# Optimization experiments

Hardware: AMD Instinct MI355X
Metric: run time of the kernel (lower is better)

## Reference

```python
import jax, jax.numpy as jnp
import numpy as np

B, S, D, K, NS = 4, 2048, 768, 8192, 2
TAU = 1.0


def setup_inputs() -> dict:
    key = jax.random.key(0)
    k1, k2, k3, k4 = jax.random.split(key, 4)
    x = jax.random.normal(k1, (B, S, D), dtype=jnp.float32)
    w_codebook = jax.random.normal(k2, (K, D), dtype=jnp.float32) * (1.0 / np.sqrt(D))
    embeddings = jax.random.normal(k3, (K, D), dtype=jnp.float32)
    # standard Gumbel(0,1) noise, one draw per (token, sample, code)
    gumbel_noise = jax.random.gumbel(k4, (B, S, NS, K), dtype=jnp.float32)
    return {"x": x, "w_codebook": w_codebook, "embeddings": embeddings,
            "gumbel_noise": gumbel_noise, "num_samples": NS}


def reference(x, w_codebook, embeddings, gumbel_noise, num_samples):
    # logits = Linear(x) without bias: [B, S, K]
    logits = jnp.einsum('bsd,kd->bsk', x, w_codebook)
    # expand over num_samples and add Gumbel noise (F.gumbel_softmax, training)
    g = (logits[:, :, None, :] + gumbel_noise) / TAU          # [B, S, NS, K]
    y_soft = jax.nn.softmax(g, axis=-1)
    # hard one-hot with straight-through estimator (hard=True, hard_p=1.0)
    idx = jnp.argmax(y_soft, axis=-1)                          # [B, S, NS]
    y_hard = jax.nn.one_hot(idx, K, dtype=y_soft.dtype)
    indices = y_hard + y_soft - jax.lax.stop_gradient(y_soft)  # [B, S, NS, K]
    # one-hot matmul == gather of codebook rows
    emb = jnp.einsum('bsnk,kd->bsnd', indices, embeddings)     # [B, S, NS, D]
    return emb, indices
```

## Files before the change

kernel.cpp:

```cpp
#include <hip/hip_runtime.h>
#include <stdint.h>

#define Bc 4
#define Sc 2048
#define Dc 768
#define Kc 8192
#define NSc 2
#define Mc (Bc*Sc)
#define EMB_ELEMS ((size_t)Mc*NSc*Dc)

typedef __attribute__((ext_vector_type(8))) __bf16 bf16x8;
typedef __attribute__((ext_vector_type(4))) float f32x4;
typedef __attribute__((ext_vector_type(4))) unsigned short u16x4;
typedef __attribute__((ext_vector_type(8))) unsigned short u16x8;

__device__ __forceinline__ unsigned short f2bf(float f){
  unsigned int u = __float_as_uint(f);
  u += 0x7FFFu + ((u >> 16) & 1u);
  return (unsigned short)(u >> 16);
}
__device__ __forceinline__ float bf2f(unsigned short h){
  return __uint_as_float(((unsigned int)h) << 16);
}

__global__ __launch_bounds__(256) void k_convert(const float4* __restrict__ x,
                                                 const float4* __restrict__ w,
                                                 u16x4* __restrict__ xb,
                                                 u16x4* __restrict__ wb){
  int i = blockIdx.x * 256 + threadIdx.x;
  float4 v = x[i];
  u16x4 o;
  o.x = f2bf(v.x); o.y = f2bf(v.y); o.z = f2bf(v.z); o.w = f2bf(v.w);
  xb[i] = o;
  v = w[i];
  o.x = f2bf(v.x); o.y = f2bf(v.y); o.z = f2bf(v.z); o.w = f2bf(v.w);
  wb[i] = o;
}

#define BM 128
#define BN 128
#define BK 32

__global__ __launch_bounds__(512, 2) void k_gemm(const unsigned short* __restrict__ xb,
                                                 const unsigned short* __restrict__ wb,
                                                 unsigned short* __restrict__ stash){
  __shared__ __align__(16) unsigned char lds[131072];

  const int tid  = threadIdx.x;
  const int lane = tid & 63;
  const int wid  = tid >> 6;
  const int wr   = wid >> 2;
  const int wc   = wid & 3;
  const int fr   = lane & 15;
  const int fq   = lane >> 4;

  const int bid = (int)blockIdx.x;
  const int swz = (bid & 7) * 128 + (bid >> 3);
  const int bm0 = (swz >> 5) * 256;
  const int bn0 = (swz & 31) * 256;

  f32x4 acc[8][4] = {};

  const int rin   = tid >> 3;
  const int kblkp = (tid & 7) ^ (rin & 7);
  const unsigned short* gsrc[8];
  unsigned dstoff[8];
  #pragma unroll
  for (int s = 0; s < 8; ++s) {
    const int isA = s >> 2;
    const int q   = s & 3;
    const int r64 = isA ? (((q & 1) << 1) | (q >> 1)) : q;
    const int grow = (isA ? bm0 : bn0) + r64 * 64 + rin;
    gsrc[s]   = (isA ? xb : wb) + (size_t)grow * Dc + kblkp * 8;
    dstoff[s] = (isA ? 0u : 32768u) + (unsigned)r64 * 8192u + (unsigned)wid * 1024u;
  }

#define ISSUE(s_, bo_) __builtin_amdgcn_global_load_lds( \
    (const __attribute__((address_space(1))) void*)gsrc[s_], \
    (__attribute__((address_space(3))) void*)&lds[(bo_) + dstoff[s_]], 16, 0, 0)

  #pragma unroll
  for (int s = 0; s < 8; ++s) ISSUE(s, 0u);
  #pragma unroll
  for (int s = 0; s < 8; ++s) gsrc[s] += 64;

  unsigned bufR = 0u, bufW = 65536u;
  const unsigned aRow = (unsigned)(wr*128 + fr) * 128u;
  const unsigned bRow = (unsigned)(wc*64  + fr) * 128u + 32768u;
  const unsigned sl0  = (unsigned)((fq       ) ^ (fr & 7)) * 16u;
  const unsigned sl1  = (unsigned)((fq + 4   ) ^ (fr & 7)) * 16u;

  for (int t = 0; t < 12; ++t) {
    const bool more = (t < 11);
    bf16x8 a[4], b0[4], b1[4];

    asm volatile("s_waitcnt vmcnt(2)" ::: "memory");
    __builtin_amdgcn_s_barrier();
    asm volatile("" ::: "memory");
    if (more) { ISSUE(0, bufW); ISSUE(1, bufW); }
    #pragma unroll
    for (int n = 0; n < 4; ++n) b0[n] = *(const bf16x8*)&lds[bufR + bRow + (unsigned)n*2048u + sl0];
    #pragma unroll
    for (int m = 0; m < 4; ++m) a[m]  = *(const bf16x8*)&lds[bufR + aRow + (unsigned)m*2048u + sl0];
    __builtin_amdgcn_s_setprio(1);
    #pragma unroll
    for (int m = 0; m < 4; ++m)
      #pragma unroll
      for (int n = 0; n < 4; ++n)
        acc[m][n] = __builtin_amdgcn_mfma_f32_16x16x32_bf16(a[m], b0[n], acc[m][n], 0, 0, 0);
    __builtin_amdgcn_s_setprio(0);

    if (more) asm volatile("s_waitcnt vmcnt(2)" ::: "memory");
    else      asm volatile("s_waitcnt vmcnt(0)" ::: "memory");
    __builtin_amdgcn_s_barrier();
    asm volatile("" ::: "memory");
    if (more) { ISSUE(2, bufW); ISSUE(3, bufW); }
    #pragma unroll
    for (int m = 0; m < 4; ++m) a[m] = *(const bf16x8*)&lds[bufR + aRow + 8192u + (unsigned)m*2048u + sl0];
    __builtin_amdgcn_s_setprio(1);
    #pragma unroll
    for (int m = 0; m < 4; ++m)
      #pragma unroll
      for (int n = 0; n < 4; ++n)
        acc[4+m][n] = __builtin_amdgcn_mfma_f32_16x16x32_bf16(a[m], b0[n], acc[4+m][n], 0, 0, 0);
    __builtin_amdgcn_s_setprio(0);

    if (more) { ISSUE(4, bufW); ISSUE(5, bufW); }
    #pragma unroll
    for (int n = 0; n < 4; ++n) b1[n] = *(const bf16x8*)&lds[bufR + bRow + (unsigned)n*2048u + sl1];
    #pragma unroll
    for (int m = 0; m < 4; ++m) a[m]  = *(const bf16x8*)&lds[bufR + aRow + (unsigned)m*2048u + sl1];
    __builtin_amdgcn_s_setprio(1);
    #pragma unroll
    for (int m = 0; m < 4; ++m)
      #pragma unroll
      for (int n = 0; n < 4; ++n)
        acc[m][n] = __builtin_amdgcn_mfma_f32_16x16x32_bf16(a[m], b1[n], acc[m][n], 0, 0, 0);
    __builtin_amdgcn_s_setprio(0);

    if (more) { ISSUE(6, bufW); ISSUE(7, bufW); }
    #pragma unroll
    for (int m = 0; m < 4; ++m) a[m] = *(const bf16x8*)&lds[bufR + aRow + 8192u + (unsigned)m*2048u + sl1];
    __builtin_amdgcn_s_setprio(1);
    #pragma unroll
    for (int m = 0; m < 4; ++m)
      #pragma unroll
      for (int n = 0; n < 4; ++n)
        acc[4+m][n] = __builtin_amdgcn_mfma_f32_16x16x32_bf16(a[m], b1[n], acc[4+m][n], 0, 0, 0);
    __builtin_amdgcn_s_setprio(0);

    bufR ^= 65536u; bufW ^= 65536u;
    if (t < 10) {
      #pragma unroll
      for (int s = 0; s < 8; ++s) gsrc[s] += 64;
    }
  }
#undef ISSUE

  unsigned short* tb16 = (unsigned short*)lds;
  #pragma unroll
  for (int h = 0; h < 2; ++h) {
    __syncthreads();
    if (wr == h) {
      #pragma unroll
      for (int m = 0; m < 8; ++m)
        #pragma unroll
        for (int n = 0; n < 4; ++n)
          #pragma unroll
          for (int r = 0; r < 4; ++r)
            tb16[(m*16 + fq*4 + r)*264 + (wc*64 + n*16 + fr)] = f2bf(acc[m][n][r]);
    }
    __syncthreads();
    #pragma unroll
    for (int i = 0; i < 8; ++i) {
      const int n = i*512 + tid;
      const int row = n >> 5, seg = n & 31;
      *(u16x8*)&stash[(size_t)(bm0 + h*128 + row) * 32768 + bn0 + seg*8] =
          *(const u16x8*)&tb16[row*264 + seg*8];
    }
  }
}

#define MARGIN 0.125f

__global__ __launch_bounds__(256) void k_select(const unsigned short* logits,
                                                const float* __restrict__ gumbel,
                                                const float* __restrict__ x,
                                                const float* __restrict__ w,
                                                const float* __restrict__ emb_tab,
                                                float* __restrict__ out_emb,
                                                float* out_ind){
  const int t   = blockIdx.x;
  const int tid = threadIdx.x;
  const int lane = tid & 63, wid = tid >> 6;

  __shared__ unsigned short Lrow[Kc];
  __shared__ float wmax[4];
  __shared__ int   cand_k[16];
  __shared__ float cand_g[16];
  __shared__ int   cand_cnt;
  __shared__ int   sel_idx[NSc];

  {
    const u16x4* src = (const u16x4*)(logits + (size_t)t * 32768);
    u16x4* dst = (u16x4*)Lrow;
    #pragma unroll
    for (int j = 0; j < 8; j++) dst[j*256 + tid] = src[j*256 + tid];
  }
  __syncthreads();

  for (int s = 0; s < NSc; ++s) {
    const float* grow = gumbel + ((size_t)t * NSc + s) * Kc;
    float4 vals[8];
    float m = -1e30f;
    #pragma unroll
    for (int j = 0; j < 8; j++) {
      float4 g4 = ((const float4*)grow)[j*256 + tid];
      u16x4 l4 = *(const u16x4*)&Lrow[j*1024 + tid*4];
      float4 v;
      v.x = bf2f(l4.x) + g4.x;
      v.y = bf2f(l4.y) + g4.y;
      v.z = bf2f(l4.z) + g4.z;
      v.w = bf2f(l4.w) + g4.w;
      vals[j] = v;
      m = fmaxf(m, fmaxf(fmaxf(v.x, v.y), fmaxf(v.z, v.w)));
    }
    #pragma unroll
    for (int off = 32; off; off >>= 1) m = fmaxf(m, __shfl_xor(m, off));
    if (lane == 0) wmax[wid] = m;
    __syncthreads();
    const float gmax = fmaxf(fmaxf(wmax[0], wmax[1]), fmaxf(wmax[2], wmax[3]));
    if (tid == 0) cand_cnt = 0;
    __syncthreads();

    const float thr = gmax - MARGIN;
    #pragma unroll
    for (int j = 0; j < 8; j++) {
      const int k0 = j*1024 + tid*4;
      float vv[4] = {vals[j].x, vals[j].y, vals[j].z, vals[j].w};
      #pragma unroll
      for (int q = 0; q < 4; q++) {
        if (vv[q] >= thr) {
          int p = atomicAdd(&cand_cnt, 1);
          if (p < 16) cand_k[p] = k0 + q;
        }
      }
    }
    __syncthreads();

    const int cnt = min(cand_cnt, 16);
    int idx;
    if (cnt == 1) {
      idx = cand_k[0];
    } else {
      for (int c = wid; c < cnt; c += 4) {
        const int kc = cand_k[c];
        const float* wr = w + (size_t)kc * Dc;
        const float* xr = x + (size_t)t * Dc;
        double accd = 0.0;
        for (int d = lane; d < Dc; d += 64) accd += (double)xr[d] * (double)wr[d];
        #pragma unroll
        for (int off = 32; off; off >>= 1) accd += __shfl_xor(accd, off);
        if (lane == 0) cand_g[c] = (float)accd + grow[kc];
      }
      __syncthreads();
      if (tid == 0) {
        float bg = -1e30f; int bk_ = Kc;
        for (int c = 0; c < cnt; c++) {
          float g = cand_g[c]; int kk = cand_k[c];
          if (g > bg || (g == bg && kk < bk_)) { bg = g; bk_ = kk; }
        }
        sel_idx[s] = bk_;
      }
      __syncthreads();
      idx = sel_idx[s];
    }
    if (cnt == 1 && tid == 0) sel_idx[s] = idx;
    __syncthreads();

    float* irow = out_ind + ((size_t)t * NSc + s) * Kc;
    #pragma unroll
    for (int j = 0; j < 8; j++) {
      const int k0 = j*1024 + tid*4;
      float4 z = {0.f, 0.f, 0.f, 0.f};
      const int d = sel_idx[s] - k0;
      if (d == 0) z.x = 1.0f; else if (d == 1) z.y = 1.0f;
      else if (d == 2) z.z = 1.0f; else if (d == 3) z.w = 1.0f;
      ((float4*)irow)[j*256 + tid] = z;
    }
    const float* er = emb_tab + (size_t)sel_idx[s] * Dc;
    float* eo = out_emb + ((size_t)t * NSc + s) * Dc;
    for (int d = tid; d < Dc; d += 256) eo[d] = er[d];
    __syncthreads();
  }
}

extern "C" void kernel_launch(void* const* d_in, const int* in_sizes, int n_in,
                              void* d_out, int out_size, void* d_ws, size_t ws_size,
                              hipStream_t stream) {
  const float* x   = (const float*)d_in[0];
  const float* w   = (const float*)d_in[1];
  const float* emb = (const float*)d_in[2];
  const float* gum = (const float*)d_in[3];

  float* out_emb = (float*)d_out;
  float* out_ind = out_emb + EMB_ELEMS;
  unsigned short* stash = (unsigned short*)out_ind;

  unsigned short* xb = (unsigned short*)d_ws;
  unsigned short* wb = xb + (size_t)Mc * Dc;

  const int n4 = (Mc * Dc) / 4;
  k_convert<<<n4 / 256, 256, 0, stream>>>((const float4*)x, (const float4*)w,
                                          (u16x4*)xb, (u16x4*)wb);
  k_gemm<<<1024, 512, 0, stream>>>(xb, wb, stash);
  k_select<<<Mc, 256, 0, stream>>>(stash, gum, x, w, emb, out_emb, out_ind);
}
```

Measured before the change: 384.5 us.

## Fuse GEMM and selection into persistent kernel with row-ready work queue

Merges the logits GEMM and the per-token gumbel selection into one persistent kernel of 256 blocks that loops over four GEMM passes. Global atomics track when all 32 column tiles of a 256-row strip are done, and blocks then pull 8-token selection chunks from a queue, so selection work overlaps the remaining GEMM tiles instead of waiting for a separate launch. This adds spin-waiting on global counters and in-order publication of finished rows. It also needs every block to be co-resident, which is a deadlock risk, and the selection now runs with 512 threads per block.

```diff
diff --git a/kernel.cpp b/kernel.cpp
--- a/kernel.cpp
+++ b/kernel.cpp
@@ -8,6 +8,7 @@
 #define NSc 2
 #define Mc (Bc*Sc)
 #define EMB_ELEMS ((size_t)Mc*NSc*Dc)
+#define MARGIN 0.125f
 
 typedef __attribute__((ext_vector_type(8))) __bf16 bf16x8;
 typedef __attribute__((ext_vector_type(4))) float f32x4;
@@ -23,10 +24,14 @@
   return __uint_as_float(((unsigned int)h) << 16);
 }
 
+#define CTL_ZERO_N 36
+
 __global__ __launch_bounds__(256) void k_convert(const float4* __restrict__ x,
                                                  const float4* __restrict__ w,
                                                  u16x4* __restrict__ xb,
-                                                 u16x4* __restrict__ wb){
+                                                 u16x4* __restrict__ wb,
+                                                 int* ctl){
+  if (blockIdx.x == 0 && threadIdx.x < CTL_ZERO_N) ctl[threadIdx.x] = 0;
   int i = blockIdx.x * 256 + threadIdx.x;
   float4 v = x[i];
   u16x4 o;
@@ -37,14 +42,32 @@
   wb[i] = o;
 }
 
-#define BM 128
-#define BN 128
-#define BK 32
-
-__global__ __launch_bounds__(512, 2) void k_gemm(const unsigned short* __restrict__ xb,
-                                                 const unsigned short* __restrict__ wb,
-                                                 unsigned short* __restrict__ stash){
+__global__ __launch_bounds__(512, 2) void k_fused(
+    const unsigned short* __restrict__ xb,
+    const unsigned short* __restrict__ wb,
+    const float* __restrict__ gumbel,
+    const float* __restrict__ x,
+    const float* __restrict__ w,
+    const float* __restrict__ emb_tab,
+    float* out_emb,
+    float* out_ind,
+    int* ctl)
+{
   __shared__ __align__(16) unsigned char lds[131072];
+  __shared__ float wmax[8];
+  __shared__ int   cand_k[16];
+  __shared__ float cand_g[16];
+  __shared__ int   cand_cnt;
+  __shared__ int   sel_idx[NSc];
+  __shared__ int   sh_c, sh_row;
+
+  int* Claimed = ctl + 0;
+  int* Avail   = ctl + 1;
+  int* NRows   = ctl + 2;
+  int* Ticket  = ctl + 4;
+  int* Rowq    = ctl + 36;
+
+  unsigned short* stash = (unsigned short*)out_ind;
 
   const int tid  = threadIdx.x;
   const int lane = tid & 63;
@@ -54,244 +77,267 @@
   const int fr   = lane & 15;
   const int fq   = lane >> 4;
 
-  const int bid = (int)blockIdx.x;
-  const int swz = (bid & 7) * 128 + (bid >> 3);
-  const int bm0 = (swz >> 5) * 256;
-  const int bn0 = (swz & 31) * 256;
-
-  f32x4 acc[8][4] = {};
-
-  const int rin   = tid >> 3;
-  const int kblkp = (tid & 7) ^ (rin & 7);
-  const unsigned short* gsrc[8];
-  unsigned dstoff[8];
-  #pragma unroll
-  for (int s = 0; s < 8; ++s) {
-    const int isA = s >> 2;
-    const int q   = s & 3;
-    const int r64 = isA ? (((q & 1) << 1) | (q >> 1)) : q;
-    const int grow = (isA ? bm0 : bn0) + r64 * 64 + rin;
-    gsrc[s]   = (isA ? xb : wb) + (size_t)grow * Dc + kblkp * 8;
-    dstoff[s] = (isA ? 0u : 32768u) + (unsigned)r64 * 8192u + (unsigned)wid * 1024u;
-  }
+  for (int pass = 0; pass < 4; ++pass) {
+    const int g   = pass * 256 + (int)blockIdx.x;
+    const int swz = (g & 7) * 128 + (g >> 3);
+    const int row = swz >> 5;
+    const int bm0 = row * 256;
+    const int bn0 = (swz & 31) * 256;
+
+    f32x4 acc[8][4] = {};
+
+    const int rin   = tid >> 3;
+    const int kblkp = (tid & 7) ^ (rin & 7);
+    const unsigned short* gsrc[8];
+    unsigned dstoff[8];
+    #pragma unroll
+    for (int s = 0; s < 8; ++s) {
+      const int isA = s >> 2;
+      const int q   = s & 3;
+      const int r64 = isA ? (((q & 1) << 1) | (q >> 1)) : q;
+      const int grow = (isA ? bm0 : bn0) + r64 * 64 + rin;
+      gsrc[s]   = (isA ? xb : wb) + (size_t)grow * Dc + kblkp * 8;
+      dstoff[s] = (isA ? 0u : 32768u) + (unsigned)r64 * 8192u + (unsigned)wid * 1024u;
+    }
 
 #define ISSUE(s_, bo_) __builtin_amdgcn_global_load_lds( \
     (const __attribute__((address_space(1))) void*)gsrc[s_], \
     (__attribute__((address_space(3))) void*)&lds[(bo_) + dstoff[s_]], 16, 0, 0)
 
-  #pragma unroll
-  for (int s = 0; s < 8; ++s) ISSUE(s, 0u);
-  #pragma unroll
-  for (int s = 0; s < 8; ++s) gsrc[s] += 64;
-
-  unsigned bufR = 0u, bufW = 65536u;
-  const unsigned aRow = (unsigned)(wr*128 + fr) * 128u;
-  const unsigned bRow = (unsigned)(wc*64  + fr) * 128u + 32768u;
-  const unsigned sl0  = (unsigned)((fq       ) ^ (fr & 7)) * 16u;
-  const unsigned sl1  = (unsigned)((fq + 4   ) ^ (fr & 7)) * 16u;
-
-  for (int t = 0; t < 12; ++t) {
-    const bool more = (t < 11);
-    bf16x8 a[4], b0[4], b1[4];
-
-    asm volatile("s_waitcnt vmcnt(2)" ::: "memory");
-    __builtin_amdgcn_s_barrier();
-    asm volatile("" ::: "memory");
-    if (more) { ISSUE(0, bufW); ISSUE(1, bufW); }
-    #pragma unroll
-    for (int n = 0; n < 4; ++n) b0[n] = *(const bf16x8*)&lds[bufR + bRow + (unsigned)n*2048u + sl0];
-    #pragma unroll
-    for (int m = 0; m < 4; ++m) a[m]  = *(const bf16x8*)&lds[bufR + aRow + (unsigned)m*2048u + sl0];
-    __builtin_amdgcn_s_setprio(1);
-    #pragma unroll
-    for (int m = 0; m < 4; ++m)
-      #pragma unroll
-      for (int n = 0; n < 4; ++n)
-        acc[m][n] = __builtin_amdgcn_mfma_f32_16x16x32_bf16(a[m], b0[n], acc[m][n], 0, 0, 0);
-    __builtin_amdgcn_s_setprio(0);
-
-    if (more) asm volatile("s_waitcnt vmcnt(2)" ::: "memory");
-    else      asm volatile("s_waitcnt vmcnt(0)" ::: "memory");
-    __builtin_amdgcn_s_barrier();
-    asm volatile("" ::: "memory");
-    if (more) { ISSUE(2, bufW); ISSUE(3, bufW); }
-    #pragma unroll
-    for (int m = 0; m < 4; ++m) a[m] = *(const bf16x8*)&lds[bufR + aRow + 8192u + (unsigned)m*2048u + sl0];
-    __builtin_amdgcn_s_setprio(1);
-    #pragma unroll
-    for (int m = 0; m < 4; ++m)
-      #pragma unroll
-      for (int n = 0; n < 4; ++n)
-        acc[4+m][n] = __builtin_amdgcn_mfma_f32_16x16x32_bf16(a[m], b0[n], acc[4+m][n], 0, 0, 0);
-    __builtin_amdgcn_s_setprio(0);
-
-    if (more) { ISSUE(4, bufW); ISSUE(5, bufW); }
-    #pragma unroll
-    for (int n = 0; n < 4; ++n) b1[n] = *(const bf16x8*)&lds[bufR + bRow + (unsigned)n*2048u + sl1];
-    #pragma unroll
-    for (int m = 0; m < 4; ++m) a[m]  = *(const bf16x8*)&lds[bufR + aRow + (unsigned)m*2048u + sl1];
-    __builtin_amdgcn_s_setprio(1);
-    #pragma unroll
-    for (int m = 0; m < 4; ++m)
-      #pragma unroll
-      for (int n = 0; n < 4; ++n)
-        acc[m][n] = __builtin_amdgcn_mfma_f32_16x16x32_bf16(a[m], b1[n], acc[m][n], 0, 0, 0);
-    __builtin_amdgcn_s_setprio(0);
-
-    if (more) { ISSUE(6, bufW); ISSUE(7, bufW); }
-    #pragma unroll
-    for (int m = 0; m < 4; ++m) a[m] = *(const bf16x8*)&lds[bufR + aRow + 8192u + (unsigned)m*2048u + sl1];
-    __builtin_amdgcn_s_setprio(1);
-    #pragma unroll
-    for (int m = 0; m < 4; ++m)
-      #pragma unroll
-      for (int n = 0; n < 4; ++n)
-        acc[4+m][n] = __builtin_amdgcn_mfma_f32_16x16x32_bf16(a[m], b1[n], acc[4+m][n], 0, 0, 0);
-    __builtin_amdgcn_s_setprio(0);
-
-    bufR ^= 65536u; bufW ^= 65536u;
-    if (t < 10) {
-      #pragma unroll
-      for (int s = 0; s < 8; ++s) gsrc[s] += 64;
-    }
-  }
-#undef ISSUE
-
-  unsigned short* tb16 = (unsigned short*)lds;
-  #pragma unroll
-  for (int h = 0; h < 2; ++h) {
-    __syncthreads();
-    if (wr == h) {
-      #pragma unroll
-      for (int m = 0; m < 8; ++m)
-        #pragma unroll
-        for (int n = 0; n < 4; ++n)
-          #pragma unroll
-          for (int r = 0; r < 4; ++r)
-            tb16[(m*16 + fq*4 + r)*264 + (wc*64 + n*16 + fr)] = f2bf(acc[m][n][r]);
-    }
     __syncthreads();
     #pragma unroll
-    for (int i = 0; i < 8; ++i) {
-      const int n = i*512 + tid;
-      const int row = n >> 5, seg = n & 31;
-      *(u16x8*)&stash[(size_t)(bm0 + h*128 + row) * 32768 + bn0 + seg*8] =
-          *(const u16x8*)&tb16[row*264 + seg*8];
-    }
-  }
-}
-
-#define MARGIN 0.125f
-
-__global__ __launch_bounds__(256) void k_select(const unsigned short* logits,
-                                                const float* __restrict__ gumbel,
-                                                const float* __restrict__ x,
-                                                const float* __restrict__ w,
-                                                const float* __restrict__ emb_tab,
-                                                float* __restrict__ out_emb,
-                                                float* out_ind){
-  const int t   = blockIdx.x;
-  const int tid = threadIdx.x;
-  const int lane = tid & 63, wid = tid >> 6;
-
-  __shared__ unsigned short Lrow[Kc];
-  __shared__ float wmax[4];
-  __shared__ int   cand_k[16];
-  __shared__ float cand_g[16];
-  __shared__ int   cand_cnt;
-  __shared__ int   sel_idx[NSc];
-
-  {
-    const u16x4* src = (const u16x4*)(logits + (size_t)t * 32768);
-    u16x4* dst = (u16x4*)Lrow;
+    for (int s = 0; s < 8; ++s) ISSUE(s, 0u);
     #pragma unroll
-    for (int j = 0; j < 8; j++) dst[j*256 + tid] = src[j*256 + tid];
-  }
-  __syncthreads();
-
-  for (int s = 0; s < NSc; ++s) {
-    const float* grow = gumbel + ((size_t)t * NSc + s) * Kc;
-    float4 vals[8];
-    float m = -1e30f;
+    for (int s = 0; s < 8; ++s) gsrc[s] += 64;
+
+    unsigned bufR = 0u, bufW = 65536u;
+    const unsigned aRow = (unsigned)(wr*128 + fr) * 128u;
+    const unsigned bRow = (unsigned)(wc*64  + fr) * 128u + 32768u;
+    const unsigned sl0  = (unsigned)((fq    ) ^ (fr & 7)) * 16u;
+    const unsigned sl1  = (unsigned)((fq + 4) ^ (fr & 7)) * 16u;
+
+    for (int t = 0; t < 12; ++t) {
+      const bool more = (t < 11);
+      bf16x8 a[4], b0[4], b1[4];
+
+      asm volatile("s_waitcnt vmcnt(2)" ::: "memory");
+      __builtin_amdgcn_s_barrier();
+      asm volatile("" ::: "memory");
+      if (more) { ISSUE(0, bufW); ISSUE(1, bufW); }
+      #pragma unroll
+      for (int n = 0; n < 4; ++n) b0[n] = *(const bf16x8*)&lds[bufR + bRow + (unsigned)n*2048u + sl0];
+      #pragma unroll
+      for (int m = 0; m < 4; ++m) a[m]  = *(const bf16x8*)&lds[bufR + aRow + (unsigned)m*2048u + sl0];
+      __builtin_amdgcn_s_setprio(1);
+      #pragma unroll
+      for (int m = 0; m < 4; ++m)
+        #pragma unroll
+        for (int n = 0; n < 4; ++n)
+          acc[m][n] = __builtin_amdgcn_mfma_f32_16x16x32_bf16(a[m], b0[n], acc[m][n], 0, 0, 0);
+      __builtin_amdgcn_s_setprio(0);
+
+      if (more) asm volatile("s_waitcnt vmcnt(2)" ::: "memory");
+      else      asm volatile("s_waitcnt vmcnt(0)" ::: "memory");
+      __builtin_amdgcn_s_barrier();
+      asm volatile("" ::: "memory");
+      if (more) { ISSUE(2, bufW); ISSUE(3, bufW); }
+      #pragma unroll
+      for (int m = 0; m < 4; ++m) a[m] = *(const bf16x8*)&lds[bufR + aRow + 8192u + (unsigned)m*2048u + sl0];
+      __builtin_amdgcn_s_setprio(1);
+      #pragma unroll
+      for (int m = 0; m < 4; ++m)
+        #pragma unroll
+        for (int n = 0; n < 4; ++n)
+          acc[4+m][n] = __builtin_amdgcn_mfma_f32_16x16x32_bf16(a[m], b0[n], acc[4+m][n], 0, 0, 0);
+      __builtin_amdgcn_s_setprio(0);
+
+      if (more) { ISSUE(4, bufW); ISSUE(5, bufW); }
+      #pragma unroll
+      for (int n = 0; n < 4; ++n) b1[n] = *(const bf16x8*)&lds[bufR + bRow + (unsigned)n*2048u + sl1];
+      #pragma unroll
+      for (int m = 0; m < 4; ++m) a[m]  = *(const bf16x8*)&lds[bufR + aRow + (unsigned)m*2048u + sl1];
+      __builtin_amdgcn_s_setprio(1);
+      #pragma unroll
+      for (int m = 0; m < 4; ++m)
+        #pragma unroll
+        for (int n = 0; n < 4; ++n)
+          acc[m][n] = __builtin_amdgcn_mfma_f32_16x16x32_bf16(a[m], b1[n], acc[m][n], 0, 0, 0);
+      __builtin_amdgcn_s_setprio(0);
+
+      if (more) { ISSUE(6, bufW); ISSUE(7, bufW); }
+      #pragma unroll
+      for (int m = 0; m < 4; ++m) a[m] = *(const bf16x8*)&lds[bufR + aRow + 8192u + (unsigned)m*2048u + sl1];
+      __builtin_amdgcn_s_setprio(1);
+      #pragma unroll
+      for (int m = 0; m < 4; ++m)
+        #pragma unroll
+        for (int n = 0; n < 4; ++n)
+          acc[4+m][n] = __builtin_amdgcn_mfma_f32_16x16x32_bf16(a[m], b1[n], acc[4+m][n], 0, 0, 0);
+      __builtin_amdgcn_s_setprio(0);
+
+      bufR ^= 65536u; bufW ^= 65536u;
+      if (t < 10) {
+        #pragma unroll
+        for (int s = 0; s < 8; ++s) gsrc[s] += 64;
+      }
+    }
+#undef ISSUE
+
+    unsigned short* tb16 = (unsigned short*)lds;
     #pragma unroll
-    for (int j = 0; j < 8; j++) {
-      float4 g4 = ((const float4*)grow)[j*256 + tid];
-      u16x4 l4 = *(const u16x4*)&Lrow[j*1024 + tid*4];
-      float4 v;
-      v.x = bf2f(l4.x) + g4.x;
-      v.y = bf2f(l4.y) + g4.y;
-      v.z = bf2f(l4.z) + g4.z;
-      v.w = bf2f(l4.w) + g4.w;
-      vals[j] = v;
-      m = fmaxf(m, fmaxf(fmaxf(v.x, v.y), fmaxf(v.z, v.w)));
-    }
-    #pragma unroll
-    for (int off = 32; off; off >>= 1) m = fmaxf(m, __shfl_xor(m, off));
-    if (lane == 0) wmax[wid] = m;
+    for (int h = 0; h < 2; ++h) {
+      __syncthreads();
+      if (wr == h) {
+        #pragma unroll
+        for (int m = 0; m < 8; ++m)
+          #pragma unroll
+          for (int n = 0; n < 4; ++n)
+            #pragma unroll
+            for (int r = 0; r < 4; ++r)
+              tb16[(m*16 + fq*4 + r)*264 + (wc*64 + n*16 + fr)] = f2bf(acc[m][n][r]);
+      }
+      __syncthreads();
+      #pragma unroll
+      for (int i = 0; i < 8; ++i) {
+        const int n = i*512 + tid;
+        const int rw = n >> 5, seg = n & 31;
+        *(u16x8*)&stash[(size_t)(bm0 + h*128 + rw) * 32768 + bn0 + seg*8] =
+            *(const u16x8*)&tb16[rw*264 + seg*8];
+      }
+    }
+
+    __threadfence();
     __syncthreads();
-    const float gmax = fmaxf(fmaxf(wmax[0], wmax[1]), fmaxf(wmax[2], wmax[3]));
-    if (tid == 0) cand_cnt = 0;
-    __syncthreads();
-
-    const float thr = gmax - MARGIN;
-    #pragma unroll
-    for (int j = 0; j < 8; j++) {
-      const int k0 = j*1024 + tid*4;
-      float vv[4] = {vals[j].x, vals[j].y, vals[j].z, vals[j].w};
-      #pragma unroll
-      for (int q = 0; q < 4; q++) {
-        if (vv[q] >= thr) {
-          int p = atomicAdd(&cand_cnt, 1);
-          if (p < 16) cand_k[p] = k0 + q;
-        }
-      }
-    }
-    __syncthreads();
-
-    const int cnt = min(cand_cnt, 16);
-    int idx;
-    if (cnt == 1) {
-      idx = cand_k[0];
-    } else {
-      for (int c = wid; c < cnt; c += 4) {
-        const int kc = cand_k[c];
-        const float* wr = w + (size_t)kc * Dc;
-        const float* xr = x + (size_t)t * Dc;
-        double accd = 0.0;
-        for (int d = lane; d < Dc; d += 64) accd += (double)xr[d] * (double)wr[d];
-        #pragma unroll
-        for (int off = 32; off; off >>= 1) accd += __shfl_xor(accd, off);
-        if (lane == 0) cand_g[c] = (float)accd + grow[kc];
-      }
+    if (tid == 0) {
+      if (atomicAdd(&Ticket[row], 1) == 31) {
+        const int pos = atomicAdd(NRows, 1);
+        Rowq[pos] = row;
+        __threadfence();
+        while (atomicAdd(Avail, 0) != pos * 256) __builtin_amdgcn_s_sleep(2);
+        atomicAdd(Avail, 256);
+      }
+    }
+
+    const bool last = (pass == 3);
+    for (;;) {
       __syncthreads();
       if (tid == 0) {
-        float bg = -1e30f; int bk_ = Kc;
-        for (int c = 0; c < cnt; c++) {
-          float g = cand_g[c]; int kk = cand_k[c];
-          if (g > bg || (g == bg && kk < bk_)) { bg = g; bk_ = kk; }
+        int c = -1;
+        if (last) {
+          c = atomicAdd(Claimed, 8);
+          if (c >= Mc) c = -1;
+        } else if (atomicAdd(Avail, 0) >= atomicAdd(Claimed, 0) + 8) {
+          c = atomicAdd(Claimed, 8);
+          if (c >= Mc) c = -1;
         }
-        sel_idx[s] = bk_;
+        if (c >= 0) {
+          while (atomicAdd(Avail, 0) < c + 8) __builtin_amdgcn_s_sleep(2);
+          __threadfence();
+          sh_row = Rowq[c >> 8];
+        }
+        sh_c = c;
       }
       __syncthreads();
-      idx = sel_idx[s];
-    }
-    if (cnt == 1 && tid == 0) sel_idx[s] = idx;
-    __syncthreads();
-
-    float* irow = out_ind + ((size_t)t * NSc + s) * Kc;
-    #pragma unroll
-    for (int j = 0; j < 8; j++) {
-      const int k0 = j*1024 + tid*4;
-      float4 z = {0.f, 0.f, 0.f, 0.f};
-      const int d = sel_idx[s] - k0;
-      if (d == 0) z.x = 1.0f; else if (d == 1) z.y = 1.0f;
-      else if (d == 2) z.z = 1.0f; else if (d == 3) z.w = 1.0f;
-      ((float4*)irow)[j*256 + tid] = z;
-    }
-    const float* er = emb_tab + (size_t)sel_idx[s] * Dc;
-    float* eo = out_emb + ((size_t)t * NSc + s) * Dc;
-    for (int d = tid; d < Dc; d += 256) eo[d] = er[d];
-    __syncthreads();
+      const int cbase = sh_c;
+      if (cbase < 0) break;
+      const int rbase = sh_row * 256 + (cbase & 255);
+
+      for (int bi = 0; bi < 8; ++bi) {
+        const int t = rbase + bi;
+        unsigned short* Lrow = (unsigned short*)lds;
+        {
+          const u16x4* src = (const u16x4*)(stash + (size_t)t * 32768);
+          u16x4* dst = (u16x4*)Lrow;
+          #pragma unroll
+          for (int j = 0; j < 4; ++j) dst[j*512 + tid] = src[j*512 + tid];
+        }
+        __syncthreads();
+
+        for (int s = 0; s < NSc; ++s) {
+          const float* grow = gumbel + ((size_t)t * NSc + s) * Kc;
+          float4 vals[4];
+          float m = -1e30f;
+          #pragma unroll
+          for (int j = 0; j < 4; ++j) {
+            float4 g4 = ((const float4*)grow)[j*512 + tid];
+            u16x4 l4 = *(const u16x4*)&Lrow[j*2048 + tid*4];
+            float4 v;
+            v.x = bf2f(l4.x) + g4.x;
+            v.y = bf2f(l4.y) + g4.y;
+            v.z = bf2f(l4.z) + g4.z;
+            v.w = bf2f(l4.w) + g4.w;
+            vals[j] = v;
+            m = fmaxf(m, fmaxf(fmaxf(v.x, v.y), fmaxf(v.z, v.w)));
+          }
+          #pragma unroll
+          for (int off = 32; off; off >>= 1) m = fmaxf(m, __shfl_xor(m, off));
+          if (lane == 0) wmax[wid] = m;
+          __syncthreads();
+          float gmax = wmax[0];
+          #pragma unroll
+          for (int q = 1; q < 8; ++q) gmax = fmaxf(gmax, wmax[q]);
+          if (tid == 0) cand_cnt = 0;
+          __syncthreads();
+
+          const float thr = gmax - MARGIN;
+          #pragma unroll
+          for (int j = 0; j < 4; ++j) {
+            const int k0 = j*2048 + tid*4;
+            float vv[4] = {vals[j].x, vals[j].y, vals[j].z, vals[j].w};
+            #pragma unroll
+            for (int q = 0; q < 4; ++q) {
+              if (vv[q] >= thr) {
+                int p = atomicAdd(&cand_cnt, 1);
+                if (p < 16) cand_k[p] = k0 + q;
+              }
+            }
+          }
+          __syncthreads();
+
+          const int cnt = min(cand_cnt, 16);
+          if (cnt == 1) {
+            if (tid == 0) sel_idx[s] = cand_k[0];
+          } else {
+            for (int c2 = wid; c2 < cnt; c2 += 8) {
+              const int kc = cand_k[c2];
+              const float* wrp = w + (size_t)kc * Dc;
+              const float* xrp = x + (size_t)t * Dc;
+              double accd = 0.0;
+              for (int d = lane; d < Dc; d += 64) accd += (double)xrp[d] * (double)wrp[d];
+              #pragma unroll
+              for (int off = 32; off; off >>= 1) accd += __shfl_xor(accd, off);
+              if (lane == 0) cand_g[c2] = (float)accd + grow[kc];
+            }
+            __syncthreads();
+            if (tid == 0) {
+              float bg = -1e30f; int bk = Kc;
+              for (int c2 = 0; c2 < cnt; ++c2) {
+                const float gg = cand_g[c2]; const int kk = cand_k[c2];
+                if (gg > bg || (gg == bg && kk < bk)) { bg = gg; bk = kk; }
+              }
+              sel_idx[s] = bk;
+            }
+          }
+          __syncthreads();
+
+          float* irow = out_ind + ((size_t)t * NSc + s) * Kc;
+          const int target = sel_idx[s];
+          #pragma unroll
+          for (int j = 0; j < 4; ++j) {
+            const int k0 = j*2048 + tid*4;
+            float4 z = {0.f, 0.f, 0.f, 0.f};
+            const int d = target - k0;
+            if (d == 0) z.x = 1.0f; else if (d == 1) z.y = 1.0f;
+            else if (d == 2) z.z = 1.0f; else if (d == 3) z.w = 1.0f;
+            ((float4*)irow)[j*512 + tid] = z;
+          }
+          const float* er = emb_tab + (size_t)target * Dc;
+          float* eo = out_emb + ((size_t)t * NSc + s) * Dc;
+          for (int d = tid; d < Dc; d += 512) eo[d] = er[d];
+          __syncthreads();
+        }
+      }
+    }
   }
 }
 
@@ -305,14 +351,13 @@
 
   float* out_emb = (float*)d_out;
   float* out_ind = out_emb + EMB_ELEMS;
-  unsigned short* stash = (unsigned short*)out_ind;
 
   unsigned short* xb = (unsigned short*)d_ws;
   unsigned short* wb = xb + (size_t)Mc * Dc;
+  int* ctl = (int*)(wb + (size_t)Kc * Dc);
 
   const int n4 = (Mc * Dc) / 4;
   k_convert<<<n4 / 256, 256, 0, stream>>>((const float4*)x, (const float4*)w,
-                                          (u16x4*)xb, (u16x4*)wb);
-  k_gemm<<<1024, 512, 0, stream>>>(xb, wb, stash);
-  k_select<<<Mc, 256, 0, stream>>>(stash, gum, x, w, emb, out_emb, out_ind);
-}
+                                          (u16x4*)xb, (u16x4*)wb, ctl);
+  k_fused<<<256, 512, 0, stream>>>(xb, wb, gum, x, w, emb, out_emb, out_ind, ctl);
+}
```

Result: slower. 973.0 us (+153.1%).
